# Optimization experiments

Measured on AMD Instinct MI355X. Metric: run time of the kernel, lower is better.

Reference implementation:

```python
import jax, jax.numpy as jnp
import numpy as np

T, N, D_IN = 24, 10000, 128
H1, H2 = 256, 128
E = 320000
OUT_DIM = 100


def _gru_params(key, d_in, h, scale=0.05):
    k1, k2, k3, k4 = jax.random.split(key, 4)
    return (jax.random.normal(k1, (3 * h, d_in), jnp.float32) * scale,
            jax.random.normal(k2, (3 * h, h), jnp.float32) * scale,
            jax.random.normal(k3, (3 * h,), jnp.float32) * scale,
            jax.random.normal(k4, (3 * h,), jnp.float32) * scale)


def setup_inputs() -> dict:
    key = jax.random.key(0)
    ks = jax.random.split(key, 8)
    x = jax.random.normal(ks[0], (T, N, D_IN), jnp.float32)
    edge_index = jax.random.randint(ks[1], (2, E), 0, N, jnp.int64)
    W_ih1, W_hh1, b_ih1, b_hh1 = _gru_params(ks[2], D_IN, H1)
    W_ih2, W_hh2, b_ih2, b_hh2 = _gru_params(ks[3], H1, H2)
    bias1 = jnp.zeros((H1,), jnp.float32)
    bias2 = jnp.zeros((H2,), jnp.float32)
    lin_W = jax.random.normal(ks[4], (OUT_DIM, H2 * N), jnp.float32) * 0.001
    lin_b = jnp.zeros((OUT_DIM,), jnp.float32)
    return dict(x=x, edge_index=edge_index,
                W_ih1=W_ih1, W_hh1=W_hh1, b_ih1=b_ih1, b_hh1=b_hh1, bias1=bias1,
                W_ih2=W_ih2, W_hh2=W_hh2, b_ih2=b_ih2, b_hh2=b_hh2, bias2=bias2,
                lin_W=lin_W, lin_b=lin_b)


def _gru(x, W_ih, W_hh, b_ih, b_hh):
    # x: (T, N, d) -> hidden states (T, N, H); torch nn.GRU semantics
    H = W_hh.shape[1]
    gi_all = jnp.einsum('tnd,hd->tnh', x, W_ih) + b_ih  # precompute input gates

    def step(h, gi):
        gh = h @ W_hh.T + b_hh
        i_r, i_z, i_n = jnp.split(gi, 3, axis=-1)
        h_r, h_z, h_n = jnp.split(gh, 3, axis=-1)
        r = jax.nn.sigmoid(i_r + h_r)
        z = jax.nn.sigmoid(i_z + h_z)
        n = jnp.tanh(i_n + r * h_n)
        h_new = (1.0 - z) * n + z * h
        return h_new, h_new

    h0 = jnp.zeros((x.shape[1], H), x.dtype)
    _, ys = jax.lax.scan(step, h0, gi_all)
    return ys


def _glstm_conv(x, edge_index, W_ih, W_hh, b_ih, b_hh, bias):
    n = x.shape[1]
    loops = jnp.arange(n, dtype=edge_index.dtype)
    ei = jnp.concatenate([edge_index, jnp.stack([loops, loops])], axis=1)
    h = _gru(x, W_ih, W_hh, b_ih, b_hh)  # (T, N, H)
    row, col = ei[0], ei[1]
    deg = jax.ops.segment_sum(jnp.ones_like(col, dtype=h.dtype), col, num_segments=n)
    dis = jnp.where(deg > 0, deg ** -0.5, 0.0)
    norm = dis[row] * dis[col]  # (E+N,)
    msgs = h[:, row, :] * norm[None, :, None]  # (T, E+N, H)
    agg = jax.ops.segment_sum(msgs.transpose(1, 0, 2), col, num_segments=n)  # (N, T, H)
    return agg.transpose(1, 0, 2) + bias


def reference(x, edge_index,
              W_ih1, W_hh1, b_ih1, b_hh1, bias1,
              W_ih2, W_hh2, b_ih2, b_hh2, bias2,
              lin_W, lin_b):
    out = _glstm_conv(x, edge_index, W_ih1, W_hh1, b_ih1, b_hh1, bias1)
    out = _glstm_conv(jax.nn.relu(out), edge_index, W_ih2, W_hh2, b_ih2, b_hh2, bias2)
    flat = out[-1].reshape(1, -1)  # (1, N*H2)
    logits = flat @ lin_W.T + lin_b
    return jax.nn.softmax(logits, axis=-1)
```

## Files before the change

### kernel.cpp

```cpp
#include <hip/hip_runtime.h>
#include <math.h>

#define TT   24
#define NN   10000
#define DIN  128
#define H1C  256
#define H2C  128
#define OUTD 100
#define FLATSZ (NN*H2C)

typedef _Float16 f16;
typedef _Float16 f16x4 __attribute__((ext_vector_type(4)));
typedef _Float16 f16x8 __attribute__((ext_vector_type(8)));
typedef float    f32x4 __attribute__((ext_vector_type(4)));
typedef int      i32x2 __attribute__((ext_vector_type(2)));

__device__ __forceinline__ float sigmoidf_(float x){ return 1.0f/(1.0f+expf(-x)); }


__global__ __launch_bounds__(256) void cast_f16_kernel(const float4* __restrict__ in,
                                                       f16x4* __restrict__ out, int n4){
  int i = blockIdx.x*256 + threadIdx.x;
  if (i < n4){
    float4 v = in[i];
    f16x4 o; o[0]=(f16)v.x; o[1]=(f16)v.y; o[2]=(f16)v.z; o[3]=(f16)v.w;
    out[i] = o;
  }
}

__global__ __launch_bounds__(256) void init_kernel(int* __restrict__ cnt, int* __restrict__ cursor,
                                                   float* __restrict__ logits, int n){
  int i = blockIdx.x*256 + threadIdx.x;
  if (i < n){ cnt[i] = 0; cursor[i] = 0; }
  if (i < OUTD) logits[i] = 0.0f;
}

__global__ __launch_bounds__(256) void count_kernel(const int* __restrict__ ei, int* __restrict__ cnt, int E){
  int e = blockIdx.x*256 + threadIdx.x;
  if (e < E) atomicAdd(&cnt[ei[E + e]], 1);
}

__global__ __launch_bounds__(256) void dis_kernel(const int* __restrict__ cnt, float* __restrict__ dis, int n){
  int i = blockIdx.x*256 + threadIdx.x;
  if (i < n) dis[i] = rsqrtf((float)(cnt[i] + 1));
}

__global__ __launch_bounds__(256) void scan_kernel(const int* __restrict__ cnt, int* __restrict__ off, int n){
  __shared__ int sums[256];
  const int tid = threadIdx.x;
  const int CH  = 40;
  const int base = tid*CH;
  int s = 0;
  for (int i = 0; i < CH; ++i){ int idx = base + i; if (idx < n) s += cnt[idx]; }
  sums[tid] = s; __syncthreads();
  for (int d = 1; d < 256; d <<= 1){
    int v = (tid >= d) ? sums[tid - d] : 0;
    __syncthreads();
    sums[tid] += v;
    __syncthreads();
  }
  int run = (tid == 0) ? 0 : sums[tid - 1];
  for (int i = 0; i < CH; ++i){
    int idx = base + i;
    if (idx < n){ off[idx] = run; run += cnt[idx]; }
  }
  if (tid == 0) off[n] = sums[255];
}

__global__ __launch_bounds__(256) void scatter_kernel(const int* __restrict__ ei, const float* __restrict__ dis,
                                                      const int* __restrict__ off, int* __restrict__ cursor,
                                                      int2* __restrict__ pe, int E){
  int e = blockIdx.x*256 + threadIdx.x;
  if (e < E){
    int r = ei[e];
    int c = ei[E + e];
    int pos = off[c] + atomicAdd(&cursor[c], 1);
    pe[pos] = make_int2(r, __float_as_int(dis[r]*dis[c]));
  }
}

__global__ __launch_bounds__(1024, 4) void gru1_chain_kernel(
    const float* __restrict__ x, const f16* __restrict__ Wih,
    const f16* __restrict__ Whh, const float* __restrict__ bih,
    const float* __restrict__ bhh, f16* __restrict__ h1all)
{
  constexpr int H  = H1C;
  constexpr int LP = H + 8;
  constexpr int XP = DIN + 8;
  __shared__ __align__(16) f16 hl[64*LP];
  __shared__ __align__(16) f16 xl[64*XP];

  const int tid  = threadIdx.x;
  const int lane = tid & 63;
  const int w    = tid >> 6;
  const int lr   = lane & 15;
  const int lk8  = (lane >> 4)*8;
  const int r0   = (lane >> 4)*4;
  const int row_base = blockIdx.x*64;

  for (int k = tid*8; k < 64*LP; k += 1024*8)
    *(f16x8*)&hl[k] = (f16x8){0,0,0,0,0,0,0,0};

  int lrow[4];
  #pragma unroll
  for (int mi = 0; mi < 4; ++mi) lrow[mi] = mi*16 + lr;

  const int col = w*16 + lr;
  int bxo[3], bho[3];
  #pragma unroll
  for (int g = 0; g < 3; ++g){
    bxo[g] = (g*H + col)*DIN + lk8;
    bho[g] = (g*H + col)*H   + lk8;
  }
  const float bR  = bih[col]       + bhh[col];
  const float bZ  = bih[H+col]     + bhh[H+col];
  const float bNi = bih[2*H+col];
  const float bNh = bhh[2*H+col];

  float hst[4][4] = {};
  __syncthreads();

  for (int t = 0; t < TT; ++t){
    {
      const float* xg = x + (size_t)t*NN*DIN;
      #pragma unroll
      for (int s = 0; s < 2; ++s){
        const int idx = s*1024 + tid;
        const int row = idx >> 5;
        const int c4  = (idx & 31)*4;
        int gr = row_base + row; if (gr >= NN) gr = NN-1;
        const f32x4 v = __builtin_nontemporal_load((const f32x4*)&xg[(size_t)gr*DIN + c4]);
        f16x4 o; o[0]=(f16)v[0]; o[1]=(f16)v[1]; o[2]=(f16)v[2]; o[3]=(f16)v[3];
        *(f16x4*)&xl[row*XP + c4] = o;
      }
    }
    __syncthreads();

    f32x4 acc[4][4] = {};

    #pragma unroll
    for (int k0 = 0; k0 < DIN; k0 += 32){
      f16x8 a[4], b[3];
      #pragma unroll
      for (int mi = 0; mi < 4; ++mi) a[mi] = *(const f16x8*)&xl[lrow[mi]*XP + k0 + lk8];
      #pragma unroll
      for (int g = 0; g < 3; ++g) b[g] = *(const f16x8*)(Wih + bxo[g] + k0);
      #pragma unroll
      for (int mi = 0; mi < 4; ++mi){
        acc[mi][0] = __builtin_amdgcn_mfma_f32_16x16x32_f16(a[mi], b[0], acc[mi][0], 0,0,0);
        acc[mi][1] = __builtin_amdgcn_mfma_f32_16x16x32_f16(a[mi], b[1], acc[mi][1], 0,0,0);
        acc[mi][2] = __builtin_amdgcn_mfma_f32_16x16x32_f16(a[mi], b[2], acc[mi][2], 0,0,0);
      }
    }
    #pragma unroll
    for (int k0 = 0; k0 < H; k0 += 32){
      f16x8 a[4], b[3];
      #pragma unroll
      for (int mi = 0; mi < 4; ++mi) a[mi] = *(const f16x8*)&hl[lrow[mi]*LP + k0 + lk8];
      #pragma unroll
      for (int g = 0; g < 3; ++g) b[g] = *(const f16x8*)(Whh + bho[g] + k0);
      #pragma unroll
      for (int mi = 0; mi < 4; ++mi){
        acc[mi][0] = __builtin_amdgcn_mfma_f32_16x16x32_f16(a[mi], b[0], acc[mi][0], 0,0,0);
        acc[mi][1] = __builtin_amdgcn_mfma_f32_16x16x32_f16(a[mi], b[1], acc[mi][1], 0,0,0);
        acc[mi][3] = __builtin_amdgcn_mfma_f32_16x16x32_f16(a[mi], b[2], acc[mi][3], 0,0,0);
      }
    }
    __syncthreads();
    #pragma unroll
    for (int mi = 0; mi < 4; ++mi){
      #pragma unroll
      for (int rr = 0; rr < 4; ++rr){
        const int rl = mi*16 + r0 + rr;
        const float rg = sigmoidf_(acc[mi][0][rr] + bR);
        const float zg = sigmoidf_(acc[mi][1][rr] + bZ);
        const float ng = tanhf(acc[mi][2][rr] + bNi + rg*(acc[mi][3][rr] + bNh));
        const float hv = (1.0f - zg)*ng + zg*hst[mi][rr];
        hst[mi][rr] = hv;
        hl[rl*LP + col] = (f16)hv;
      }
    }
    __syncthreads();
    f16* ho = h1all + ((size_t)t*NN + row_base)*H;
    #pragma unroll
    for (int c = 0; c < 2; ++c){
      const int idx = c*1024 + tid;
      const int row = idx >> 5, seg = idx & 31;
      if (row_base + row < NN)
        __builtin_nontemporal_store(*(const f16x8*)&hl[row*LP + seg*8],
                                    (f16x8*)&ho[(size_t)row*H + seg*8]);
    }
  }
}

__global__ __launch_bounds__(512, 2) void gru2_chain_kernel(
    const f16* __restrict__ x2all, const f16* __restrict__ Wih,
    const f16* __restrict__ Whh, const float* __restrict__ bih,
    const float* __restrict__ bhh, float* __restrict__ h2fin)
{
  constexpr int H   = H2C;
  constexpr int KX  = H1C;
  constexpr int LP  = H + 8;
  constexpr int X2P = KX + 8;
  __shared__ __align__(16) f16 hl[64*LP];
  __shared__ __align__(16) f16 x2l[64*X2P];

  const int tid  = threadIdx.x;
  const int lane = tid & 63;
  const int w    = tid >> 6;
  const int lr   = lane & 15;
  const int lk8  = (lane >> 4)*8;
  const int r0   = (lane >> 4)*4;
  const int row_base = blockIdx.x*64;

  for (int k = tid*8; k < 64*LP; k += 512*8)
    *(f16x8*)&hl[k] = (f16x8){0,0,0,0,0,0,0,0};

  int lrow[4];
  #pragma unroll
  for (int mi = 0; mi < 4; ++mi) lrow[mi] = mi*16 + lr;

  const int col = w*16 + lr;
  int bxo[3], bho[3];
  #pragma unroll
  for (int g = 0; g < 3; ++g){
    bxo[g] = (g*H + col)*KX + lk8;
    bho[g] = (g*H + col)*H  + lk8;
  }
  const float bR  = bih[col]       + bhh[col];
  const float bZ  = bih[H+col]     + bhh[H+col];
  const float bNi = bih[2*H+col];
  const float bNh = bhh[2*H+col];

  float hst[4][4] = {};
  __syncthreads();

  for (int t = 0; t < TT; ++t){
    {
      const f16* xg = x2all + (size_t)t*NN*KX;
      #pragma unroll
      for (int s = 0; s < 4; ++s){
        const int idx = s*512 + tid;
        const int row = idx >> 5;
        const int sg  = (idx & 31)*8;
        int gr = row_base + row; if (gr >= NN) gr = NN-1;
        f16x8 v = __builtin_nontemporal_load((const f16x8*)&xg[(size_t)gr*KX + sg]);
        *(f16x8*)&x2l[row*X2P + sg] = v;
      }
    }
    __syncthreads();

    f32x4 acc[4][4] = {};

    #pragma unroll
    for (int k0 = 0; k0 < KX; k0 += 32){
      f16x8 a[4], b[3];
      #pragma unroll
      for (int mi = 0; mi < 4; ++mi) a[mi] = *(const f16x8*)&x2l[lrow[mi]*X2P + k0 + lk8];
      #pragma unroll
      for (int g = 0; g < 3; ++g) b[g] = *(const f16x8*)(Wih + bxo[g] + k0);
      #pragma unroll
      for (int mi = 0; mi < 4; ++mi){
        acc[mi][0] = __builtin_amdgcn_mfma_f32_16x16x32_f16(a[mi], b[0], acc[mi][0], 0,0,0);
        acc[mi][1] = __builtin_amdgcn_mfma_f32_16x16x32_f16(a[mi], b[1], acc[mi][1], 0,0,0);
        acc[mi][2] = __builtin_amdgcn_mfma_f32_16x16x32_f16(a[mi], b[2], acc[mi][2], 0,0,0);
      }
    }
    #pragma unroll
    for (int k0 = 0; k0 < H; k0 += 32){
      f16x8 a[4], b[3];
      #pragma unroll
      for (int mi = 0; mi < 4; ++mi) a[mi] = *(const f16x8*)&hl[lrow[mi]*LP + k0 + lk8];
      #pragma unroll
      for (int g = 0; g < 3; ++g) b[g] = *(const f16x8*)(Whh + bho[g] + k0);
      #pragma unroll
      for (int mi = 0; mi < 4; ++mi){
        acc[mi][0] = __builtin_amdgcn_mfma_f32_16x16x32_f16(a[mi], b[0], acc[mi][0], 0,0,0);
        acc[mi][1] = __builtin_amdgcn_mfma_f32_16x16x32_f16(a[mi], b[1], acc[mi][1], 0,0,0);
        acc[mi][3] = __builtin_amdgcn_mfma_f32_16x16x32_f16(a[mi], b[2], acc[mi][3], 0,0,0);
      }
    }
    __syncthreads();
    #pragma unroll
    for (int mi = 0; mi < 4; ++mi){
      #pragma unroll
      for (int rr = 0; rr < 4; ++rr){
        const int rl = mi*16 + r0 + rr;
        const int growu = row_base + rl;
        const float rg = sigmoidf_(acc[mi][0][rr] + bR);
        const float zg = sigmoidf_(acc[mi][1][rr] + bZ);
        const float ng = tanhf(acc[mi][2][rr] + bNi + rg*(acc[mi][3][rr] + bNh));
        const float hv = (1.0f - zg)*ng + zg*hst[mi][rr];
        hst[mi][rr] = hv;
        hl[rl*LP + col] = (f16)hv;
        if (t == TT-1 && growu < NN)
          h2fin[(size_t)growu*H + col] = hv;
      }
    }
    __syncthreads();
  }
}

__global__ __launch_bounds__(512) void conv1_kernel(
    const f16* __restrict__ hall, const int2* __restrict__ pe,
    const int* __restrict__ off, const float* __restrict__ dis,
    const float* __restrict__ bias, f16* __restrict__ outall)
{
  const int b   = blockIdx.x;
  const int xcd = b & 7;
  const int v   = b >> 3;
  const int tq  = v / 1250;
  const int t   = xcd + 8*tq;
  const int i   = (v - tq*1250)*8 + (threadIdx.x >> 6);
  const int f   = threadIdx.x & 63;
  const f16x4* hp = (const f16x4*)(hall + (size_t)t*NN*H1C);
  const float d = dis[i];
  const f16x4 sv = hp[(size_t)i*64 + f];
  float a0 = d*d*(float)sv[0];
  float a1 = d*d*(float)sv[1];
  float a2 = d*d*(float)sv[2];
  float a3 = d*d*(float)sv[3];
  int e = off[i]; const int e2 = off[i+1];
  const i32x2* pev = (const i32x2*)pe;
  for (; e + 8 <= e2; e += 8){
    i32x2 q[8];
    #pragma unroll
    for (int u = 0; u < 8; ++u) q[u] = __builtin_nontemporal_load(&pev[e+u]);
    #pragma unroll
    for (int u = 0; u < 8; ++u){
      const float wq = __int_as_float(q[u][1]);
      const f16x4 vv = hp[(size_t)q[u][0]*64 + f];
      a0 += wq*(float)vv[0]; a1 += wq*(float)vv[1];
      a2 += wq*(float)vv[2]; a3 += wq*(float)vv[3];
    }
  }
  for (; e < e2; ++e){
    const int2 q = pe[e];
    const float wq = __int_as_float(q.y);
    const f16x4 vv = hp[(size_t)q.x*64 + f];
    a0 += wq*(float)vv[0]; a1 += wq*(float)vv[1];
    a2 += wq*(float)vv[2]; a3 += wq*(float)vv[3];
  }
  const float4 bb = ((const float4*)bias)[f];
  a0 = fmaxf(a0 + bb.x, 0.0f);
  a1 = fmaxf(a1 + bb.y, 0.0f);
  a2 = fmaxf(a2 + bb.z, 0.0f);
  a3 = fmaxf(a3 + bb.w, 0.0f);
  f16x4 o; o[0]=(f16)a0; o[1]=(f16)a1; o[2]=(f16)a2; o[3]=(f16)a3;
  __builtin_nontemporal_store(o, (f16x4*)(outall + (size_t)t*NN*H1C) + (size_t)i*64 + f);
}

__global__ __launch_bounds__(64) void conv2_kernel(
    const float* __restrict__ h, const int2* __restrict__ pe,
    const int* __restrict__ off, const float* __restrict__ dis,
    const float* __restrict__ bias, float* __restrict__ out)
{
  const int i = blockIdx.x;
  const int f = threadIdx.x;
  const float2* hp = (const float2*)h;
  const float d = dis[i];
  const float2 sv = hp[(size_t)i*64 + f];
  float a0 = d*d*sv.x;
  float a1 = d*d*sv.y;
  int e = off[i]; const int e2 = off[i+1];
  for (; e + 4 <= e2; e += 4){
    int2 q[4];
    #pragma unroll
    for (int u = 0; u < 4; ++u) q[u] = pe[e+u];
    #pragma unroll
    for (int u = 0; u < 4; ++u){
      const float wq = __int_as_float(q[u].y);
      const float2 vv = hp[(size_t)q[u].x*64 + f];
      a0 += wq*vv.x; a1 += wq*vv.y;
    }
  }
  for (; e < e2; ++e){
    const int2 q = pe[e];
    const float wq = __int_as_float(q.y);
    const float2 vv = hp[(size_t)q.x*64 + f];
    a0 += wq*vv.x; a1 += wq*vv.y;
  }
  const float2 bb = ((const float2*)bias)[f];
  ((float2*)out)[(size_t)i*64 + f] = make_float2(a0 + bb.x, a1 + bb.y);
}

__global__ __launch_bounds__(256) void dense_kernel(const float* __restrict__ flat,
    const float* __restrict__ linW, float* __restrict__ logits)
{
  const int j   = blockIdx.x;
  const int tid = threadIdx.x;
  const int Q4  = FLATSZ/4;
  const int CH4 = Q4/64;
  const int s4  = blockIdx.y*CH4;
  const int e4  = s4 + CH4;
  const f32x4* w4 = (const f32x4*)&linW[(size_t)j*FLATSZ];
  const float4* f4 = (const float4*)flat;
  float part = 0.0f;
  for (int i = s4 + tid; i < e4; i += 256){
    const f32x4 a = __builtin_nontemporal_load(&w4[i]);
    const float4 b = f4[i];
    part += a[0]*b.x + a[1]*b.y + a[2]*b.z + a[3]*b.w;
  }
  __shared__ float red[256];
  red[tid] = part; __syncthreads();
  for (int s = 128; s > 0; s >>= 1){
    if (tid < s) red[tid] += red[tid + s];
    __syncthreads();
  }
  if (tid == 0) atomicAdd(&logits[j], red[0]);
}

__global__ __launch_bounds__(128) void softmax_kernel(const float* __restrict__ logits,
    const float* __restrict__ linb, float* __restrict__ out)
{
  __shared__ float red[128];
  const int tid = threadIdx.x;
  const float v = (tid < OUTD) ? logits[tid] + linb[tid] : -INFINITY;
  red[tid] = v; __syncthreads();
  for (int s = 64; s > 0; s >>= 1){
    if (tid < s) red[tid] = fmaxf(red[tid], red[tid + s]);
    __syncthreads();
  }
  const float mx = red[0]; __syncthreads();
  const float e = (tid < OUTD) ? expf(v - mx) : 0.0f;
  red[tid] = e; __syncthreads();
  for (int s = 64; s > 0; s >>= 1){
    if (tid < s) red[tid] += red[tid + s];
    __syncthreads();
  }
  const float inv = 1.0f/red[0];
  if (tid < OUTD) out[tid] = e*inv;
}


extern "C" void kernel_launch(void* const* d_in, const int* in_sizes, int n_in,
                              void* d_out, int out_size, void* d_ws, size_t ws_size,
                              hipStream_t stream)
{
  const float* x     = (const float*)d_in[0];
  const int*   ei    = (const int*)  d_in[1];
  const float* W_ih1 = (const float*)d_in[2];
  const float* W_hh1 = (const float*)d_in[3];
  const float* b_ih1 = (const float*)d_in[4];
  const float* b_hh1 = (const float*)d_in[5];
  const float* bias1 = (const float*)d_in[6];
  const float* W_ih2 = (const float*)d_in[7];
  const float* W_hh2 = (const float*)d_in[8];
  const float* b_ih2 = (const float*)d_in[9];
  const float* b_hh2 = (const float*)d_in[10];
  const float* bias2 = (const float*)d_in[11];
  const float* lin_W = (const float*)d_in[12];
  const float* lin_b = (const float*)d_in[13];
  float* out = (float*)d_out;
  const int E = in_sizes[1]/2;
  (void)n_in; (void)out_size; (void)ws_size;

  char* p = (char*)d_ws;
  auto alloc = [&](size_t bytes)->void* {
    void* r = (void*)p;
    p += (bytes + 255) & ~(size_t)255;
    return r;
  };
  int*   cnt    = (int*)  alloc((size_t)NN*4);
  int*   cursor = (int*)  alloc((size_t)NN*4);
  int*   offs   = (int*)  alloc((size_t)(NN+1)*4);
  float* dis    = (float*)alloc((size_t)NN*4);
  int2*  pe     = (int2*) alloc((size_t)E*8);
  f16*   h1all  = (f16*)  alloc((size_t)TT*NN*H1C*2);
  f16*   x2all  = (f16*)  alloc((size_t)TT*NN*H1C*2);
  float* h2fin  = (float*)alloc((size_t)NN*H2C*4);
  float* out2   = (float*)alloc((size_t)NN*H2C*4);
  f16*   wih1h  = (f16*)  alloc((size_t)3*H1C*DIN*2);
  f16*   whh1h  = (f16*)  alloc((size_t)3*H1C*H1C*2);
  f16*   wih2h  = (f16*)  alloc((size_t)3*H2C*H1C*2);
  f16*   whh2h  = (f16*)  alloc((size_t)3*H2C*H2C*2);
  float* logits = (float*)alloc((size_t)OUTD*4);

  init_kernel   <<<(NN+255)/256, 256, 0, stream>>>(cnt, cursor, logits, NN);
  count_kernel  <<<(E+255)/256, 256, 0, stream>>>(ei, cnt, E);
  dis_kernel    <<<(NN+255)/256, 256, 0, stream>>>(cnt, dis, NN);
  scan_kernel   <<<1, 256, 0, stream>>>(cnt, offs, NN);
  scatter_kernel<<<(E+255)/256, 256, 0, stream>>>(ei, dis, offs, cursor, pe, E);

  cast_f16_kernel<<<((3*H1C*DIN/4)+255)/256, 256, 0, stream>>>((const float4*)W_ih1, (f16x4*)wih1h, 3*H1C*DIN/4);
  cast_f16_kernel<<<((3*H1C*H1C/4)+255)/256, 256, 0, stream>>>((const float4*)W_hh1, (f16x4*)whh1h, 3*H1C*H1C/4);
  cast_f16_kernel<<<((3*H2C*H1C/4)+255)/256, 256, 0, stream>>>((const float4*)W_ih2, (f16x4*)wih2h, 3*H2C*H1C/4);
  cast_f16_kernel<<<((3*H2C*H2C/4)+255)/256, 256, 0, stream>>>((const float4*)W_hh2, (f16x4*)whh2h, 3*H2C*H2C/4);

  const int CB = (NN + 63)/64;

  gru1_chain_kernel<<<CB, 1024, 0, stream>>>(x, wih1h, whh1h, b_ih1, b_hh1, h1all);

  conv1_kernel<<<24*NN/8, 512, 0, stream>>>(h1all, pe, offs, dis, bias1, x2all);

  gru2_chain_kernel<<<CB, 512, 0, stream>>>(x2all, wih2h, whh2h, b_ih2, b_hh2, h2fin);

  conv2_kernel<<<NN, 64, 0, stream>>>(h2fin, pe, offs, dis, bias2, out2);
  dense_kernel<<<dim3(OUTD, 64), 256, 0, stream>>>(out2, lin_W, logits);
  softmax_kernel<<<1, 128, 0, stream>>>(logits, lin_b, out);
}
```

Baseline: 1.723 ms.

## Prefetch next timestep's input into registers with double-buffered LDS in GRU chains

Both GRU chain kernels now issue the global load for timestep t+1's input into registers right after storing timestep t's input into one of two LDS buffers. The load latency can then overlap with the MFMA work of the current step instead of stalling at its start. The cost is more LDS (the input tile is doubled) and extra live registers, which may lower occupancy given the tight launch bounds.

```diff
diff --git a/kernel.cpp b/kernel.cpp
--- a/kernel.cpp
+++ b/kernel.cpp
@@ -88,7 +88,7 @@
   constexpr int LP = H + 8;
   constexpr int XP = DIN + 8;
   __shared__ __align__(16) f16 hl[64*LP];
-  __shared__ __align__(16) f16 xl[64*XP];
+  __shared__ __align__(16) f16 xl[2][64*XP];
 
   const int tid  = threadIdx.x;
   const int lane = tid & 63;
@@ -117,24 +117,39 @@
   const float bNi = bih[2*H+col];
   const float bNh = bhh[2*H+col];
 
+  int srow[2], sc4[2], soff[2];
+  #pragma unroll
+  for (int s = 0; s < 2; ++s){
+    const int idx = s*1024 + tid;
+    srow[s] = idx >> 5;
+    sc4[s]  = (idx & 31)*4;
+    int gr = row_base + srow[s]; if (gr >= NN) gr = NN-1;
+    soff[s] = gr*DIN + sc4[s];
+  }
+
   float hst[4][4] = {};
+  f32x4 xreg[2];
+  #pragma unroll
+  for (int s = 0; s < 2; ++s)
+    xreg[s] = __builtin_nontemporal_load((const f32x4*)&x[soff[s]]);
   __syncthreads();
 
   for (int t = 0; t < TT; ++t){
+    f16* xbuf = xl[t&1];
+    #pragma unroll
+    for (int s = 0; s < 2; ++s){
+      f16x4 o; o[0]=(f16)xreg[s][0]; o[1]=(f16)xreg[s][1]; o[2]=(f16)xreg[s][2]; o[3]=(f16)xreg[s][3];
+      *(f16x4*)&xbuf[srow[s]*XP + sc4[s]] = o;
+    }
+    __syncthreads();
+
     {
-      const float* xg = x + (size_t)t*NN*DIN;
-      #pragma unroll
-      for (int s = 0; s < 2; ++s){
-        const int idx = s*1024 + tid;
-        const int row = idx >> 5;
-        const int c4  = (idx & 31)*4;
-        int gr = row_base + row; if (gr >= NN) gr = NN-1;
-        const f32x4 v = __builtin_nontemporal_load((const f32x4*)&xg[(size_t)gr*DIN + c4]);
-        f16x4 o; o[0]=(f16)v[0]; o[1]=(f16)v[1]; o[2]=(f16)v[2]; o[3]=(f16)v[3];
-        *(f16x4*)&xl[row*XP + c4] = o;
-      }
-    }
-    __syncthreads();
+      const int tn = (t+1 < TT) ? t+1 : t;
+      const float* xg = x + (size_t)tn*NN*DIN;
+      #pragma unroll
+      for (int s = 0; s < 2; ++s)
+        xreg[s] = __builtin_nontemporal_load((const f32x4*)&xg[soff[s]]);
+    }
 
     f32x4 acc[4][4] = {};
 
@@ -142,7 +157,7 @@
     for (int k0 = 0; k0 < DIN; k0 += 32){
       f16x8 a[4], b[3];
       #pragma unroll
-      for (int mi = 0; mi < 4; ++mi) a[mi] = *(const f16x8*)&xl[lrow[mi]*XP + k0 + lk8];
+      for (int mi = 0; mi < 4; ++mi) a[mi] = *(const f16x8*)&xbuf[lrow[mi]*XP + k0 + lk8];
       #pragma unroll
       for (int g = 0; g < 3; ++g) b[g] = *(const f16x8*)(Wih + bxo[g] + k0);
       #pragma unroll
@@ -203,7 +218,7 @@
   constexpr int LP  = H + 8;
   constexpr int X2P = KX + 8;
   __shared__ __align__(16) f16 hl[64*LP];
-  __shared__ __align__(16) f16 x2l[64*X2P];
+  __shared__ __align__(16) f16 x2l[2][64*X2P];
 
   const int tid  = threadIdx.x;
   const int lane = tid & 63;
@@ -232,23 +247,37 @@
   const float bNi = bih[2*H+col];
   const float bNh = bhh[2*H+col];
 
+  int srow[4], ssg[4], soff[4];
+  #pragma unroll
+  for (int s = 0; s < 4; ++s){
+    const int idx = s*512 + tid;
+    srow[s] = idx >> 5;
+    ssg[s]  = (idx & 31)*8;
+    int gr = row_base + srow[s]; if (gr >= NN) gr = NN-1;
+    soff[s] = gr*KX + ssg[s];
+  }
+
   float hst[4][4] = {};
+  f16x8 xreg[4];
+  #pragma unroll
+  for (int s = 0; s < 4; ++s)
+    xreg[s] = __builtin_nontemporal_load((const f16x8*)&x2all[soff[s]]);
   __syncthreads();
 
   for (int t = 0; t < TT; ++t){
+    f16* xbuf = x2l[t&1];
+    #pragma unroll
+    for (int s = 0; s < 4; ++s)
+      *(f16x8*)&xbuf[srow[s]*X2P + ssg[s]] = xreg[s];
+    __syncthreads();
+
     {
-      const f16* xg = x2all + (size_t)t*NN*KX;
-      #pragma unroll
-      for (int s = 0; s < 4; ++s){
-        const int idx = s*512 + tid;
-        const int row = idx >> 5;
-        const int sg  = (idx & 31)*8;
-        int gr = row_base + row; if (gr >= NN) gr = NN-1;
-        f16x8 v = __builtin_nontemporal_load((const f16x8*)&xg[(size_t)gr*KX + sg]);
-        *(f16x8*)&x2l[row*X2P + sg] = v;
-      }
-    }
-    __syncthreads();
+      const int tn = (t+1 < TT) ? t+1 : t;
+      const f16* xg = x2all + (size_t)tn*NN*KX;
+      #pragma unroll
+      for (int s = 0; s < 4; ++s)
+        xreg[s] = __builtin_nontemporal_load((const f16x8*)&xg[soff[s]]);
+    }
 
     f32x4 acc[4][4] = {};
 
@@ -256,7 +285,7 @@
     for (int k0 = 0; k0 < KX; k0 += 32){
       f16x8 a[4], b[3];
       #pragma unroll
-      for (int mi = 0; mi < 4; ++mi) a[mi] = *(const f16x8*)&x2l[lrow[mi]*X2P + k0 + lk8];
+      for (int mi = 0; mi < 4; ++mi) a[mi] = *(const f16x8*)&xbuf[lrow[mi]*X2P + k0 + lk8];
       #pragma unroll
       for (int g = 0; g < 3; ++g) b[g] = *(const f16x8*)(Wih + bxo[g] + k0);
       #pragma unroll
```

Measured after the change: 1.655 ms. 1.04x faster.
